# Kernel tuning notes

Measured on AMD Instinct MI355X. Metric: run time of the kernel, lower is better.

Reference implementation:

```python
import jax, jax.numpy as jnp
import numpy as np

T = 1_000_000
DT = 1e-3  # uniform t_eval spacing; integration horizon t in [0, 1000)


def setup_inputs() -> dict:
    return {
        "t_eval": jnp.arange(T, dtype=jnp.float32) * DT,
        "x0": jnp.array([0.15, 0.08, 0.05], dtype=jnp.float32),
        "log_eps": jnp.float32(-2.0),
        "log_delta": jnp.float32(-0.5),
        "theta": jnp.full((3,), 0.1, dtype=jnp.float32),
        "readout_w": jnp.eye(3, dtype=jnp.float32),   # nn.init.eye_
        "readout_b": jnp.zeros((3,), dtype=jnp.float32),
    }


def _build_W(log_eps, log_delta, dtype):
    # W[i,j] = 0 if i==j; -1+eps if i==(j+1)%3; else -1-delta
    eps = jnp.exp(log_eps)
    delta = jnp.exp(log_delta)
    eye = jnp.eye(3, dtype=dtype)
    cyc = jnp.array([[0, 0, 1], [1, 0, 0], [0, 1, 0]], dtype=dtype)  # i == (j+1)%3
    return cyc * (-1.0 + eps) + (1.0 - eye - cyc) * (-1.0 - delta)


def _integrate(t_eval, x0, log_eps, log_delta, theta):
    """Dormand-Prince 5(4) stages, one fixed step per t_eval interval (dopri5 tableau)."""
    W = _build_W(log_eps, log_delta, x0.dtype)

    def f(x):  # autonomous CTLN RHS: -x + relu(W x + theta)
        return -x + jax.nn.relu(W @ x + theta)

    def step(x, dt):
        k1 = f(x)
        k2 = f(x + dt * (1.0 / 5.0 * k1))
        k3 = f(x + dt * (3.0 / 40.0 * k1 + 9.0 / 40.0 * k2))
        k4 = f(x + dt * (44.0 / 45.0 * k1 - 56.0 / 15.0 * k2 + 32.0 / 9.0 * k3))
        k5 = f(x + dt * (19372.0 / 6561.0 * k1 - 25360.0 / 2187.0 * k2
                         + 64448.0 / 6561.0 * k3 - 212.0 / 729.0 * k4))
        k6 = f(x + dt * (9017.0 / 3168.0 * k1 - 355.0 / 33.0 * k2
                         + 46732.0 / 5247.0 * k3 + 49.0 / 176.0 * k4
                         - 5103.0 / 18656.0 * k5))
        x_new = x + dt * (35.0 / 384.0 * k1 + 500.0 / 1113.0 * k3
                          + 125.0 / 192.0 * k4 - 2187.0 / 6784.0 * k5
                          + 11.0 / 84.0 * k6)
        return x_new, x_new

    dts = jnp.diff(t_eval)                       # [T-1]
    _, xs = jax.lax.scan(step, x0, dts)          # [T-1, 3]
    return jnp.concatenate([x0[None, :], xs], axis=0)  # [T, 3]


def reference(t_eval, x0, log_eps, log_delta, theta, readout_w, readout_b):
    traj = _integrate(t_eval, x0, log_eps, log_delta, theta)  # [T, 3]
    pred = traj @ readout_w.T + readout_b                      # Linear(3,3)
    return traj, pred
```

## Files before the change

### kernel.cpp

```cpp
#include <hip/hip_runtime.h>
#include <math.h>


#define C21 (1.0/5.0)
#define C31 (3.0/40.0)
#define C32 (9.0/40.0)
#define C41 (44.0/45.0)
#define C42 (-56.0/15.0)
#define C43 (32.0/9.0)
#define C51 (19372.0/6561.0)
#define C52 (-25360.0/2187.0)
#define C53 (64448.0/6561.0)
#define C54 (-212.0/729.0)
#define C61 (9017.0/3168.0)
#define C62 (-355.0/33.0)
#define C63 (46732.0/5247.0)
#define C64 (49.0/176.0)
#define C65 (-5103.0/18656.0)
#define B1  (35.0/384.0)
#define B3  (500.0/1113.0)
#define B4  (125.0/192.0)
#define B5  (-2187.0/6784.0)
#define B6  (11.0/84.0)

template <typename T> struct MapT { T A[9]; T b[3]; };

template <typename T>
__device__ inline void map_identity(MapT<T>& m) {
#pragma unroll
  for (int i = 0; i < 9; ++i) m.A[i] = T(0);
  m.A[0] = m.A[4] = m.A[8] = T(1);
  m.b[0] = m.b[1] = m.b[2] = T(0);
}

template <typename T>
__device__ inline void map_compose(MapT<T>& out, const MapT<T>& m2, const MapT<T>& m1) {
#pragma unroll
  for (int r = 0; r < 3; ++r) {
#pragma unroll
    for (int c = 0; c < 3; ++c)
      out.A[r*3+c] = m2.A[r*3+0]*m1.A[0+c] + m2.A[r*3+1]*m1.A[3+c] + m2.A[r*3+2]*m1.A[6+c];
    out.b[r] = m2.A[r*3+0]*m1.b[0] + m2.A[r*3+1]*m1.b[1] + m2.A[r*3+2]*m1.b[2] + m2.b[r];
  }
}

template <typename T>
__device__ inline void map_apply(const MapT<T>& m, const T x[3], T y[3]) {
#pragma unroll
  for (int r = 0; r < 3; ++r)
    y[r] = m.A[r*3+0]*x[0] + m.A[r*3+1]*x[1] + m.A[r*3+2]*x[2] + m.b[r];
}

template <typename T>
__device__ inline MapT<T> map_shfl_up(const MapT<T>& m, int off) {
  MapT<T> r;
#pragma unroll
  for (int i = 0; i < 9; ++i) r.A[i] = __shfl_up(m.A[i], off, 64);
#pragma unroll
  for (int i = 0; i < 3; ++i) r.b[i] = __shfl_up(m.b[i], off, 64);
  return r;
}

template <typename T, bool RECORD>
__device__ inline void stage_k(const T z[3], const T th[3],
                               T wa, T wb, T g[3], T k[3]) {
  T y0 = fma(wa, z[2], fma(wb, z[1], th[0]));
  T y1 = fma(wa, z[0], fma(wb, z[2], th[1]));
  T y2 = fma(wa, z[1], fma(wb, z[0], th[2]));
  if (RECORD) {
    g[0] = (y0 > T(0)) ? T(1) : T(0);
    g[1] = (y1 > T(0)) ? T(1) : T(0);
    g[2] = (y2 > T(0)) ? T(1) : T(0);
  }
  k[0] = y0 * g[0] - z[0];
  k[1] = y1 * g[1] - z[1];
  k[2] = y2 * g[2] - z[2];
}

template <typename T, bool RECORD>
__device__ inline void dopri_eval(const T v[3], const T th[3], T dt,
                                  T wa, T wb, T G[6][3], T out[3]) {
  T k1[3], k2[3], k3[3], k4[3], k5[3], k6[3], z[3];
  stage_k<T, RECORD>(v, th, wa, wb, G[0], k1);
  const T d21 = dt * T(C21);
#pragma unroll
  for (int c = 0; c < 3; ++c) z[c] = fma(d21, k1[c], v[c]);
  stage_k<T, RECORD>(z, th, wa, wb, G[1], k2);
#pragma unroll
  for (int c = 0; c < 3; ++c) z[c] = fma(dt, fma(T(C31), k1[c], T(C32) * k2[c]), v[c]);
  stage_k<T, RECORD>(z, th, wa, wb, G[2], k3);
#pragma unroll
  for (int c = 0; c < 3; ++c)
    z[c] = fma(dt, fma(T(C41), k1[c], fma(T(C42), k2[c], T(C43) * k3[c])), v[c]);
  stage_k<T, RECORD>(z, th, wa, wb, G[3], k4);
#pragma unroll
  for (int c = 0; c < 3; ++c)
    z[c] = fma(dt, fma(T(C51), k1[c], fma(T(C52), k2[c], fma(T(C53), k3[c], T(C54) * k4[c]))), v[c]);
  stage_k<T, RECORD>(z, th, wa, wb, G[4], k5);
#pragma unroll
  for (int c = 0; c < 3; ++c)
    z[c] = fma(dt, fma(T(C61), k1[c], fma(T(C62), k2[c], fma(T(C63), k3[c], fma(T(C64), k4[c], T(C65) * k5[c])))), v[c]);
  stage_k<T, RECORD>(z, th, wa, wb, G[5], k6);
#pragma unroll
  for (int c = 0; c < 3; ++c)
    out[c] = fma(dt, fma(T(B1), k1[c], fma(T(B3), k3[c], fma(T(B4), k4[c], fma(T(B5), k5[c], T(B6) * k6[c])))), v[c]);
}

template <typename T>
__device__ inline void build_map(const T xo[3], T dt, T wa, T wb,
                                 const T th[3], MapT<T>& m) {
  T G[6][3], dump[3];
  dopri_eval<T, true>(xo, th, dt, wa, wb, G, dump);
  const T z3[3] = {T(0), T(0), T(0)};
  dopri_eval<T, false>(z3, th, dt, wa, wb, G, m.b);
  T e[3], col[3];
#pragma unroll
  for (int j = 0; j < 3; ++j) {
    e[0] = T(0); e[1] = T(0); e[2] = T(0); e[j] = T(1);
    dopri_eval<T, false>(e, z3, dt, wa, wb, G, col);
    m.A[0 + j] = col[0];
    m.A[3 + j] = col[1];
    m.A[6 + j] = col[2];
  }
}


__global__ void k_dts(const float* __restrict__ t, float* __restrict__ dts, int S) {
  int i = blockIdx.x * blockDim.x + threadIdx.x;
  if (i < S) dts[i] = t[i + 1] - t[i];
}

__global__ void k_coarse(const float* __restrict__ x0f,
                         const float* __restrict__ le, const float* __restrict__ ld,
                         const float* __restrict__ thf,
                         float* __restrict__ cst, int NC, float dtc) {
  if (threadIdx.x != 0 || blockIdx.x != 0) return;
  const float a = -1.f + expf(le[0]);
  const float b = -1.f - expf(ld[0]);
  const float t0 = thf[0], t1 = thf[1], t2 = thf[2];
  float x = x0f[0], y = x0f[1], z = x0f[2];
  cst[0] = x; cst[1] = y; cst[2] = z;
  const float dt = dtc, dth = 0.5f * dtc, dt6 = dtc * (1.f / 6.f);
#define RHSF(px, py, pz, kx, ky, kz)                      \
  do {                                                    \
    float y0_ = fmaf(a, (pz), fmaf(b, (py), t0));         \
    float y1_ = fmaf(a, (px), fmaf(b, (pz), t1));         \
    float y2_ = fmaf(a, (py), fmaf(b, (px), t2));         \
    (kx) = fmaxf(y0_, 0.f) - (px);                        \
    (ky) = fmaxf(y1_, 0.f) - (py);                        \
    (kz) = fmaxf(y2_, 0.f) - (pz);                        \
  } while (0)
  for (int i = 1; i <= NC; ++i) {
    float k1x,k1y,k1z,k2x,k2y,k2z,k3x,k3y,k3z,k4x,k4y,k4z,zx,zy,zz;
    RHSF(x, y, z, k1x, k1y, k1z);
    zx = fmaf(dth, k1x, x); zy = fmaf(dth, k1y, y); zz = fmaf(dth, k1z, z);
    RHSF(zx, zy, zz, k2x, k2y, k2z);
    zx = fmaf(dth, k2x, x); zy = fmaf(dth, k2y, y); zz = fmaf(dth, k2z, z);
    RHSF(zx, zy, zz, k3x, k3y, k3z);
    zx = fmaf(dt, k3x, x); zy = fmaf(dt, k3y, y); zz = fmaf(dt, k3z, z);
    RHSF(zx, zy, zz, k4x, k4y, k4z);
    x = fmaf(dt6, k1x + 2.f*k2x + 2.f*k3x + k4x, x);
    y = fmaf(dt6, k1y + 2.f*k2y + 2.f*k3y + k4y, y);
    z = fmaf(dt6, k1z + 2.f*k2z + 2.f*k3z + k4z, z);
    cst[3*i] = x; cst[3*i+1] = y; cst[3*i+2] = z;
  }
#undef RHSF
}

__global__ void k_interp(const float* __restrict__ t_eval, const float* __restrict__ st,
                         float* __restrict__ out, int T, float h, int nstates) {
  int n = blockIdx.x * blockDim.x + threadIdx.x;
  if (n >= T) return;
  float u = t_eval[n] / h;
  int j = (int)u;
  if (j < 0) j = 0;
  if (j > nstates - 2) j = nstates - 2;
  float f = u - (float)j;
#pragma unroll
  for (int c = 0; c < 3; ++c) {
    float a = st[3*j + c], b = st[3*(j+1) + c];
    out[3*n + c] = a + f * (b - a);
  }
}


#define FT 256
#define FT_LOG2 8
#define FCH 8
#define BT 512

template <typename T>
__global__ __launch_bounds__(FT) void k_upscan(
    const float* __restrict__ src, const float* __restrict__ dts,
    const float* __restrict__ le, const float* __restrict__ ld,
    const float* __restrict__ thf,
    MapT<T>* __restrict__ lpre, MapT<T>* __restrict__ btot, int S, int NG1) {
  __shared__ MapT<T> wtot[FT / 64];
  const int t = threadIdx.x;
  const int lane = t & 63, wid = t >> 6;
  const int g = blockIdx.x * FT + t;
  const T wa = (T)(-1.0 + exp((double)le[0]));
  const T wb = (T)(-1.0 - exp((double)ld[0]));
  const T th[3] = {(T)thf[0], (T)thf[1], (T)thf[2]};

  MapT<T> run, mp, tmp;
  map_identity(run);
  if (g < NG1) {
    for (int s = 0; s < FCH; ++s) {
      int n = g * FCH + s;
      if (n >= S) break;
      T xo[3] = {(T)src[3*n], (T)src[3*n+1], (T)src[3*n+2]};
      build_map(xo, (T)dts[n], wa, wb, th, mp);
      map_compose(tmp, mp, run);
      run = tmp;
    }
  }
#pragma unroll
  for (int off = 1; off < 64; off <<= 1) {
    MapT<T> nb = map_shfl_up(run, off);
    MapT<T> comp; map_compose(comp, run, nb);
    if (lane >= off) run = comp;
  }
  if (lane == 63) wtot[wid] = run;
  __syncthreads();
  MapT<T> wpre; map_identity(wpre);
  for (int w = 0; w < wid; ++w) { MapT<T> t2; map_compose(t2, wtot[w], wpre); wpre = t2; }

  MapT<T> excl = map_shfl_up(run, 1);
  if (lane == 0) map_identity(excl);
  MapT<T> P; map_compose(P, excl, wpre);
  lpre[g] = P;
  if (t == FT - 1) { MapT<T> bt; map_compose(bt, run, wpre); btot[blockIdx.x] = bt; }
}

template <typename T>
__global__ __launch_bounds__(BT) void k_bscan(const MapT<T>* __restrict__ btot,
                                              MapT<T>* __restrict__ bpre, int NB) {
  __shared__ MapT<T> wtot[BT / 64];
  const int t = threadIdx.x;
  const int lane = t & 63, wid = t >> 6;
  MapT<T> run;
  if (t < NB) run = btot[t]; else map_identity(run);
#pragma unroll
  for (int off = 1; off < 64; off <<= 1) {
    MapT<T> nb = map_shfl_up(run, off);
    MapT<T> comp; map_compose(comp, run, nb);
    if (lane >= off) run = comp;
  }
  if (lane == 63) wtot[wid] = run;
  __syncthreads();
  MapT<T> wpre; map_identity(wpre);
  for (int w = 0; w < wid; ++w) { MapT<T> t2; map_compose(t2, wtot[w], wpre); wpre = t2; }
  MapT<T> excl = map_shfl_up(run, 1);
  if (lane == 0) map_identity(excl);
  if (t < NB) { MapT<T> P; map_compose(P, excl, wpre); bpre[t] = P; }
}

template <typename T>
__global__ __launch_bounds__(FT) void k_apply2(
    const float* __restrict__ src, float* __restrict__ dst,
    const float* __restrict__ dts,
    const MapT<T>* __restrict__ lpre, const MapT<T>* __restrict__ bpre,
    const float* __restrict__ le, const float* __restrict__ ld,
    const float* __restrict__ thf, const float* __restrict__ x0f, int S, int NG1) {
  const int g = blockIdx.x * blockDim.x + threadIdx.x;
  if (g >= NG1) return;
  const T wa = (T)(-1.0 + exp((double)le[0]));
  const T wb = (T)(-1.0 - exp((double)ld[0]));
  const T th[3] = {(T)thf[0], (T)thf[1], (T)thf[2]};
  const T x0d[3] = {(T)x0f[0], (T)x0f[1], (T)x0f[2]};

  MapT<T> P;
  map_compose(P, lpre[g], bpre[g >> FT_LOG2]);
  T x[3], xn[3];
  map_apply(P, x0d, x);
  if (g == 0) { dst[0] = x0f[0]; dst[1] = x0f[1]; dst[2] = x0f[2]; }
  MapT<T> mp;
  for (int s = 0; s < FCH; ++s) {
    int n = g * FCH + s;
    if (n >= S) break;
    T xo[3] = {(T)src[3*n], (T)src[3*n+1], (T)src[3*n+2]};
    build_map(xo, (T)dts[n], wa, wb, th, mp);
    map_apply(mp, x, xn);
    x[0] = xn[0]; x[1] = xn[1]; x[2] = xn[2];
    dst[3*(n+1)]   = (float)x[0];
    dst[3*(n+1)+1] = (float)x[1];
    dst[3*(n+1)+2] = (float)x[2];
  }
}

__global__ __launch_bounds__(256) void k_polish(
    const float* __restrict__ src, float* __restrict__ dst,
    const float* __restrict__ dts,
    const float* __restrict__ le, const float* __restrict__ ld,
    const float* __restrict__ thf, const float* __restrict__ x0f, int S, int NG1) {
  const int g = blockIdx.x * blockDim.x + threadIdx.x;
  if (g >= NG1) return;
  const double wa = -1.0 + exp((double)le[0]);
  const double wb = -1.0 - exp((double)ld[0]);
  const double th[3] = {(double)thf[0], (double)thf[1], (double)thf[2]};
  const int n0 = g * FCH;
  double x[3];
  if (g == 0) {
    x[0] = (double)x0f[0]; x[1] = (double)x0f[1]; x[2] = (double)x0f[2];
    dst[0] = x0f[0]; dst[1] = x0f[1]; dst[2] = x0f[2];
  } else {
    x[0] = (double)src[3*n0]; x[1] = (double)src[3*n0+1]; x[2] = (double)src[3*n0+2];
  }
  double G[6][3], xn[3];
  for (int s = 0; s < FCH; ++s) {
    int n = n0 + s;
    if (n >= S) break;
    dopri_eval<double, true>(x, th, (double)dts[n], wa, wb, G, xn);
    x[0] = xn[0]; x[1] = xn[1]; x[2] = xn[2];
    dst[3*(n+1)]   = (float)x[0];
    dst[3*(n+1)+1] = (float)x[1];
    dst[3*(n+1)+2] = (float)x[2];
  }
}

__global__ void k_readout(const float* __restrict__ traj, const float* __restrict__ w,
                          const float* __restrict__ bvec, float* __restrict__ pred, int T) {
  const float w00=w[0],w01=w[1],w02=w[2];
  const float w10=w[3],w11=w[4],w12=w[5];
  const float w20=w[6],w21=w[7],w22=w[8];
  const float b0=bvec[0], b1=bvec[1], b2=bvec[2];
  for (int i = blockIdx.x * blockDim.x + threadIdx.x; i < T;
       i += gridDim.x * blockDim.x) {
    const float x0 = traj[3*i], x1 = traj[3*i+1], x2 = traj[3*i+2];
    pred[3*i]   = fmaf(w00,x0, fmaf(w01,x1, fmaf(w02,x2, b0)));
    pred[3*i+1] = fmaf(w10,x0, fmaf(w11,x1, fmaf(w12,x2, b1)));
    pred[3*i+2] = fmaf(w20,x0, fmaf(w21,x1, fmaf(w22,x2, b2)));
  }
}


extern "C" void kernel_launch(void* const* d_in, const int* in_sizes, int n_in,
                              void* d_out, int out_size, void* d_ws, size_t ws_size,
                              hipStream_t stream) {
  const float* t_eval    = (const float*)d_in[0];
  const float* x0        = (const float*)d_in[1];
  const float* log_eps   = (const float*)d_in[2];
  const float* log_delta = (const float*)d_in[3];
  const float* theta     = (const float*)d_in[4];
  const float* readout_w = (const float*)d_in[5];
  const float* readout_b = (const float*)d_in[6];

  const int T   = in_sizes[0];
  const int S   = T - 1;
  const int NG1 = (S + FCH - 1) / FCH;
  const int NB  = (NG1 + FT - 1) / FT;

  const float  DTS_SEED = 0.45f;
  const int    NSEED    = (int)(((double)S * 1e-3) / (double)DTS_SEED) + 2;

  float* trajh = (float*)d_out;
  float* predh = trajh + (size_t)3 * T;

  char* w = (char*)d_ws;
  float* dts    = (float*)w;  w += (((size_t)S * 4) + 255) & ~(size_t)255;
  float* seedst = (float*)w;  w += (((size_t)3 * (NSEED + 1) * 4) + 255) & ~(size_t)255;
  MapT<float>* lpre = (MapT<float>*)w; w += (((size_t)NB * FT * sizeof(MapT<float>)) + 255) & ~(size_t)255;
  MapT<float>* btot = (MapT<float>*)w; w += (((size_t)BT * sizeof(MapT<float>)) + 255) & ~(size_t)255;
  MapT<float>* bpre = (MapT<float>*)w;

  k_dts<<<(S + 255) / 256, 256, 0, stream>>>(t_eval, dts, S);
  k_coarse<<<1, 64, 0, stream>>>(x0, log_eps, log_delta, theta, seedst, NSEED, DTS_SEED);
  k_interp<<<(T + 255) / 256, 256, 0, stream>>>(t_eval, seedst, predh, T,
                                                DTS_SEED, NSEED + 1);

  for (int it = 0; it < 4; ++it) {
    const float* src = (it % 2 == 0) ? predh : trajh;
    float*       dst = (it % 2 == 0) ? trajh : predh;
    k_upscan<float><<<NB, FT, 0, stream>>>(src, dts, log_eps, log_delta, theta,
                                           lpre, btot, S, NG1);
    k_bscan<float><<<1, BT, 0, stream>>>(btot, bpre, NB);
    k_apply2<float><<<(NG1 + FT - 1) / FT, FT, 0, stream>>>(src, dst, dts, lpre, bpre,
                                                            log_eps, log_delta, theta,
                                                            x0, S, NG1);
  }

  k_polish<<<(NG1 + 255) / 256, 256, 0, stream>>>(predh, trajh, dts, log_eps,
                                                  log_delta, theta, x0, S, NG1);

  k_readout<<<2048, 256, 0, stream>>>(trajh, readout_w, readout_b, predh, T);
}
```

Measured before the change: 627.2 us.

## Fuse Newton-scan iterations into one cooperative kernel over group start states

Replaces the per-iteration upscan, bscan and apply kernel trio with a single cooperative kernel that uses grid.sync between the block-level scan and the cross-block scan. Only per-group start states are carried between iterations; the full trajectory is no longer written each pass, since each thread re-walks its chunk from its start state. The chunk size per thread goes from 8 to 16, step sizes are computed inline from t_eval, and the readout is fused into the final double-precision polish kernel. A multi-kernel fallback path runs if the cooperative launch fails. The cost is more recomputation per thread and a dependence on all blocks being co-resident.

```diff
diff --git a/kernel.cpp b/kernel.cpp
--- a/kernel.cpp
+++ b/kernel.cpp
@@ -1,5 +1,8 @@
 #include <hip/hip_runtime.h>
+#include <hip/hip_cooperative_groups.h>
 #include <math.h>
+
+namespace cg = cooperative_groups;
 
 
 #define C21 (1.0/5.0)
@@ -23,18 +26,21 @@
 #define B5  (-2187.0/6784.0)
 #define B6  (11.0/84.0)
 
-template <typename T> struct MapT { T A[9]; T b[3]; };
-
-template <typename T>
-__device__ inline void map_identity(MapT<T>& m) {
-#pragma unroll
-  for (int i = 0; i < 9; ++i) m.A[i] = T(0);
-  m.A[0] = m.A[4] = m.A[8] = T(1);
-  m.b[0] = m.b[1] = m.b[2] = T(0);
-}
-
-template <typename T>
-__device__ inline void map_compose(MapT<T>& out, const MapT<T>& m2, const MapT<T>& m1) {
+#define FT 256
+#define FT_LOG2 8
+#define FCH 16
+#define NITER 4
+
+struct MapF { float A[9]; float b[3]; };
+
+__device__ inline void map_identity(MapF& m) {
+#pragma unroll
+  for (int i = 0; i < 9; ++i) m.A[i] = 0.f;
+  m.A[0] = m.A[4] = m.A[8] = 1.f;
+  m.b[0] = m.b[1] = m.b[2] = 0.f;
+}
+
+__device__ inline void map_compose(MapF& out, const MapF& m2, const MapF& m1) {
 #pragma unroll
   for (int r = 0; r < 3; ++r) {
 #pragma unroll
@@ -44,16 +50,14 @@
   }
 }
 
-template <typename T>
-__device__ inline void map_apply(const MapT<T>& m, const T x[3], T y[3]) {
+__device__ inline void map_apply(const MapF& m, const float x[3], float y[3]) {
 #pragma unroll
   for (int r = 0; r < 3; ++r)
     y[r] = m.A[r*3+0]*x[0] + m.A[r*3+1]*x[1] + m.A[r*3+2]*x[2] + m.b[r];
 }
 
-template <typename T>
-__device__ inline MapT<T> map_shfl_up(const MapT<T>& m, int off) {
-  MapT<T> r;
+__device__ inline MapF map_shfl_up(const MapF& m, int off) {
+  MapF r;
 #pragma unroll
   for (int i = 0; i < 9; ++i) r.A[i] = __shfl_up(m.A[i], off, 64);
 #pragma unroll
@@ -106,29 +110,71 @@
     out[c] = fma(dt, fma(T(B1), k1[c], fma(T(B3), k3[c], fma(T(B4), k4[c], fma(T(B5), k5[c], T(B6) * k6[c])))), v[c]);
 }
 
-template <typename T>
-__device__ inline void build_map(const T xo[3], T dt, T wa, T wb,
-                                 const T th[3], MapT<T>& m) {
-  T G[6][3], dump[3];
-  dopri_eval<T, true>(xo, th, dt, wa, wb, G, dump);
-  const T z3[3] = {T(0), T(0), T(0)};
-  dopri_eval<T, false>(z3, th, dt, wa, wb, G, m.b);
-  T e[3], col[3];
+__device__ inline void build_map_step(float x[3], float dt, float wa, float wb,
+                                      const float th[3], MapF& m) {
+  float G[6][3], xn[3];
+  dopri_eval<float, true>(x, th, dt, wa, wb, G, xn);
+  const float z3[3] = {0.f, 0.f, 0.f};
+  dopri_eval<float, false>(z3, th, dt, wa, wb, G, m.b);
+  float e[3], col[3];
 #pragma unroll
   for (int j = 0; j < 3; ++j) {
-    e[0] = T(0); e[1] = T(0); e[2] = T(0); e[j] = T(1);
-    dopri_eval<T, false>(e, z3, dt, wa, wb, G, col);
+    e[0] = 0.f; e[1] = 0.f; e[2] = 0.f; e[j] = 1.f;
+    dopri_eval<float, false>(e, z3, dt, wa, wb, G, col);
     m.A[0 + j] = col[0];
     m.A[3 + j] = col[1];
     m.A[6 + j] = col[2];
   }
-}
-
-
-__global__ void k_dts(const float* __restrict__ t, float* __restrict__ dts, int S) {
-  int i = blockIdx.x * blockDim.x + threadIdx.x;
-  if (i < S) dts[i] = t[i + 1] - t[i];
-}
+  x[0] = xn[0]; x[1] = xn[1]; x[2] = xn[2];
+}
+
+__device__ inline void block_scan(MapF run, MapF& P, MapF& tot,
+                                  MapF* wtot, int lane, int wid) {
+#pragma unroll
+  for (int off = 1; off < 64; off <<= 1) {
+    MapF nb = map_shfl_up(run, off);
+    MapF c; map_compose(c, run, nb);
+    if (lane >= off) run = c;
+  }
+  __syncthreads();
+  if (lane == 63) wtot[wid] = run;
+  __syncthreads();
+  MapF wpre; map_identity(wpre);
+  for (int w = 0; w < wid; ++w) { MapF t2; map_compose(t2, wtot[w], wpre); wpre = t2; }
+  MapF excl = map_shfl_up(run, 1);
+  if (lane == 0) map_identity(excl);
+  map_compose(P, excl, wpre);
+  map_compose(tot, run, wpre);
+}
+
+__device__ inline void group_walk(float xs[3], const float dtg[FCH],
+                                  float wa, float wb, const float th[3],
+                                  MapF& run) {
+  map_identity(run);
+  MapF mp, tmp;
+  float x[3] = {xs[0], xs[1], xs[2]};
+#pragma unroll
+  for (int s = 0; s < FCH; ++s) {
+    build_map_step(x, dtg[s], wa, wb, th, mp);
+    map_compose(tmp, mp, run);
+    run = tmp;
+  }
+}
+
+__device__ inline void load_dtg(const float* __restrict__ t_eval, int n0, int T,
+                                float dtg[FCH], float& tv0) {
+  int i0 = n0 > T - 1 ? T - 1 : n0;
+  tv0 = t_eval[i0];
+  float prev = tv0;
+#pragma unroll
+  for (int s = 1; s <= FCH; ++s) {
+    int idx = n0 + s; if (idx > T - 1) idx = T - 1;
+    float c = t_eval[idx];
+    dtg[s - 1] = c - prev;
+    prev = c;
+  }
+}
+
 
 __global__ void k_coarse(const float* __restrict__ x0f,
                          const float* __restrict__ le, const float* __restrict__ ld,
@@ -167,171 +213,203 @@
 #undef RHSF
 }
 
-__global__ void k_interp(const float* __restrict__ t_eval, const float* __restrict__ st,
-                         float* __restrict__ out, int T, float h, int nstates) {
-  int n = blockIdx.x * blockDim.x + threadIdx.x;
-  if (n >= T) return;
-  float u = t_eval[n] / h;
+__global__ __launch_bounds__(FT) void k_mega(
+    const float* __restrict__ t_eval, const float* __restrict__ seedst,
+    const float* __restrict__ x0f,
+    const float* __restrict__ le, const float* __restrict__ ld,
+    const float* __restrict__ thf,
+    float* __restrict__ gstart,
+    MapF* __restrict__ btot, MapF* __restrict__ bpre,
+    int S, int T, int NG1, int NB, float hseed, int nstates) {
+  cg::grid_group grid = cg::this_grid();
+  __shared__ MapF wtot[FT / 64];
+
+  const int t = threadIdx.x;
+  const int lane = t & 63, wid = t >> 6;
+  const int g = blockIdx.x * FT + t;
+  const bool active = (g < NG1);
+  const int n0 = g * FCH;
+
+  const float wa = -1.f + expf(le[0]);
+  const float wb = -1.f - expf(ld[0]);
+  const float th[3] = {thf[0], thf[1], thf[2]};
+  const float x0d[3] = {x0f[0], x0f[1], x0f[2]};
+
+  float dtg[FCH];
+  float xs[3] = {0.f, 0.f, 0.f};
+  if (active) {
+    float tv0;
+    load_dtg(t_eval, n0, T, dtg, tv0);
+    float u = tv0 / hseed;
+    int j = (int)u;
+    if (j < 0) j = 0;
+    if (j > nstates - 2) j = nstates - 2;
+    float f = u - (float)j;
+#pragma unroll
+    for (int c = 0; c < 3; ++c) {
+      float a0 = seedst[3*j + c], b0 = seedst[3*(j+1) + c];
+      xs[c] = a0 + f * (b0 - a0);
+    }
+  } else {
+#pragma unroll
+    for (int s = 0; s < FCH; ++s) dtg[s] = 0.f;
+  }
+  if (g == 0) { xs[0] = x0d[0]; xs[1] = x0d[1]; xs[2] = x0d[2]; }
+
+  for (int it = 0; it < NITER; ++it) {
+    MapF run;
+    if (active) group_walk(xs, dtg, wa, wb, th, run);
+    else map_identity(run);
+
+    MapF P, tot;
+    block_scan(run, P, tot, wtot, lane, wid);
+    if (t == FT - 1) btot[blockIdx.x] = tot;
+    grid.sync();
+
+    if (blockIdx.x == 0) {
+      MapF rb;
+      if (t < NB) rb = btot[t]; else map_identity(rb);
+      MapF Pb, totb;
+      block_scan(rb, Pb, totb, wtot, lane, wid);
+      if (t < NB) bpre[t] = Pb;
+    }
+    grid.sync();
+
+    {
+      MapF bp = bpre[blockIdx.x];
+      MapF Pn; map_compose(Pn, P, bp);
+      float ns[3]; map_apply(Pn, x0d, ns);
+      if (active && g != 0) { xs[0] = ns[0]; xs[1] = ns[1]; xs[2] = ns[2]; }
+    }
+  }
+
+  if (active) {
+    gstart[3*g]   = xs[0];
+    gstart[3*g+1] = xs[1];
+    gstart[3*g+2] = xs[2];
+  }
+}
+
+__global__ __launch_bounds__(256) void k_polish(
+    const float* __restrict__ t_eval, const float* __restrict__ gstart,
+    const float* __restrict__ x0f,
+    const float* __restrict__ le, const float* __restrict__ ld,
+    const float* __restrict__ thf,
+    const float* __restrict__ row, const float* __restrict__ rob,
+    float* __restrict__ traj, float* __restrict__ pred, int S, int T, int NG1) {
+  const int g = blockIdx.x * blockDim.x + threadIdx.x;
+  if (g >= NG1) return;
+  const int n0 = g * FCH;
+  float dtg[FCH]; float tv0;
+  load_dtg(t_eval, n0, T, dtg, tv0);
+
+  const double wa = -1.0 + exp((double)le[0]);
+  const double wb = -1.0 - exp((double)ld[0]);
+  const double th[3] = {(double)thf[0], (double)thf[1], (double)thf[2]};
+  const float w00 = row[0], w01 = row[1], w02 = row[2];
+  const float w10 = row[3], w11 = row[4], w12 = row[5];
+  const float w20 = row[6], w21 = row[7], w22 = row[8];
+  const float b0 = rob[0], b1 = rob[1], b2 = rob[2];
+
+  double x[3];
+  if (g == 0) {
+    x[0] = (double)x0f[0]; x[1] = (double)x0f[1]; x[2] = (double)x0f[2];
+    float a0 = x0f[0], a1 = x0f[1], a2 = x0f[2];
+    traj[0] = a0; traj[1] = a1; traj[2] = a2;
+    pred[0] = fmaf(w00, a0, fmaf(w01, a1, fmaf(w02, a2, b0)));
+    pred[1] = fmaf(w10, a0, fmaf(w11, a1, fmaf(w12, a2, b1)));
+    pred[2] = fmaf(w20, a0, fmaf(w21, a1, fmaf(w22, a2, b2)));
+  } else {
+    x[0] = (double)gstart[3*g]; x[1] = (double)gstart[3*g+1]; x[2] = (double)gstart[3*g+2];
+  }
+
+  double G[6][3], xn[3];
+#pragma unroll
+  for (int s = 0; s < FCH; ++s) {
+    dopri_eval<double, true>(x, th, (double)dtg[s], wa, wb, G, xn);
+    x[0] = xn[0]; x[1] = xn[1]; x[2] = xn[2];
+    int n = n0 + s;
+    if (n < S) {
+      float a0 = (float)x[0], a1 = (float)x[1], a2 = (float)x[2];
+      traj[3*(n+1)]   = a0;
+      traj[3*(n+1)+1] = a1;
+      traj[3*(n+1)+2] = a2;
+      pred[3*(n+1)]   = fmaf(w00, a0, fmaf(w01, a1, fmaf(w02, a2, b0)));
+      pred[3*(n+1)+1] = fmaf(w10, a0, fmaf(w11, a1, fmaf(w12, a2, b1)));
+      pred[3*(n+1)+2] = fmaf(w20, a0, fmaf(w21, a1, fmaf(w22, a2, b2)));
+    }
+  }
+}
+
+
+__global__ void k_start0(const float* __restrict__ t_eval,
+                         const float* __restrict__ seedst,
+                         const float* __restrict__ x0f,
+                         float* __restrict__ gs, int T, int NG1,
+                         float hseed, int nstates) {
+  int g = blockIdx.x * blockDim.x + threadIdx.x;
+  if (g >= NG1) return;
+  if (g == 0) { gs[0] = x0f[0]; gs[1] = x0f[1]; gs[2] = x0f[2]; return; }
+  int n0 = g * FCH; if (n0 > T - 1) n0 = T - 1;
+  float u = t_eval[n0] / hseed;
   int j = (int)u;
   if (j < 0) j = 0;
   if (j > nstates - 2) j = nstates - 2;
   float f = u - (float)j;
 #pragma unroll
   for (int c = 0; c < 3; ++c) {
-    float a = st[3*j + c], b = st[3*(j+1) + c];
-    out[3*n + c] = a + f * (b - a);
-  }
-}
-
-
-#define FT 256
-#define FT_LOG2 8
-#define FCH 8
-#define BT 512
-
-template <typename T>
-__global__ __launch_bounds__(FT) void k_upscan(
-    const float* __restrict__ src, const float* __restrict__ dts,
+    float a0 = seedst[3*j + c], b0 = seedst[3*(j+1) + c];
+    gs[3*g + c] = a0 + f * (b0 - a0);
+  }
+}
+
+__global__ __launch_bounds__(FT) void k_up_fb(
+    const float* __restrict__ t_eval, const float* __restrict__ gs,
     const float* __restrict__ le, const float* __restrict__ ld,
     const float* __restrict__ thf,
-    MapT<T>* __restrict__ lpre, MapT<T>* __restrict__ btot, int S, int NG1) {
-  __shared__ MapT<T> wtot[FT / 64];
-  const int t = threadIdx.x;
-  const int lane = t & 63, wid = t >> 6;
+    MapF* __restrict__ lpre, MapF* __restrict__ btot, int T, int NG1) {
+  __shared__ MapF wtot[FT / 64];
+  const int t = threadIdx.x, lane = t & 63, wid = t >> 6;
   const int g = blockIdx.x * FT + t;
-  const T wa = (T)(-1.0 + exp((double)le[0]));
-  const T wb = (T)(-1.0 - exp((double)ld[0]));
-  const T th[3] = {(T)thf[0], (T)thf[1], (T)thf[2]};
-
-  MapT<T> run, mp, tmp;
-  map_identity(run);
-  if (g < NG1) {
-    for (int s = 0; s < FCH; ++s) {
-      int n = g * FCH + s;
-      if (n >= S) break;
-      T xo[3] = {(T)src[3*n], (T)src[3*n+1], (T)src[3*n+2]};
-      build_map(xo, (T)dts[n], wa, wb, th, mp);
-      map_compose(tmp, mp, run);
-      run = tmp;
-    }
-  }
-#pragma unroll
-  for (int off = 1; off < 64; off <<= 1) {
-    MapT<T> nb = map_shfl_up(run, off);
-    MapT<T> comp; map_compose(comp, run, nb);
-    if (lane >= off) run = comp;
-  }
-  if (lane == 63) wtot[wid] = run;
-  __syncthreads();
-  MapT<T> wpre; map_identity(wpre);
-  for (int w = 0; w < wid; ++w) { MapT<T> t2; map_compose(t2, wtot[w], wpre); wpre = t2; }
-
-  MapT<T> excl = map_shfl_up(run, 1);
-  if (lane == 0) map_identity(excl);
-  MapT<T> P; map_compose(P, excl, wpre);
-  lpre[g] = P;
-  if (t == FT - 1) { MapT<T> bt; map_compose(bt, run, wpre); btot[blockIdx.x] = bt; }
-}
-
-template <typename T>
-__global__ __launch_bounds__(BT) void k_bscan(const MapT<T>* __restrict__ btot,
-                                              MapT<T>* __restrict__ bpre, int NB) {
-  __shared__ MapT<T> wtot[BT / 64];
-  const int t = threadIdx.x;
-  const int lane = t & 63, wid = t >> 6;
-  MapT<T> run;
+  const bool active = (g < NG1);
+  const float wa = -1.f + expf(le[0]);
+  const float wb = -1.f - expf(ld[0]);
+  const float th[3] = {thf[0], thf[1], thf[2]};
+  MapF run;
+  if (active) {
+    float dtg[FCH]; float tv0;
+    load_dtg(t_eval, g * FCH, T, dtg, tv0);
+    float xs[3] = {gs[3*g], gs[3*g+1], gs[3*g+2]};
+    group_walk(xs, dtg, wa, wb, th, run);
+  } else map_identity(run);
+  MapF P, tot;
+  block_scan(run, P, tot, wtot, lane, wid);
+  if (active) lpre[g] = P;
+  if (t == FT - 1) btot[blockIdx.x] = tot;
+}
+
+__global__ __launch_bounds__(FT) void k_bscan_fb(const MapF* __restrict__ btot,
+                                                 MapF* __restrict__ bpre, int NB) {
+  __shared__ MapF wtot[FT / 64];
+  const int t = threadIdx.x, lane = t & 63, wid = t >> 6;
+  MapF run;
   if (t < NB) run = btot[t]; else map_identity(run);
-#pragma unroll
-  for (int off = 1; off < 64; off <<= 1) {
-    MapT<T> nb = map_shfl_up(run, off);
-    MapT<T> comp; map_compose(comp, run, nb);
-    if (lane >= off) run = comp;
-  }
-  if (lane == 63) wtot[wid] = run;
-  __syncthreads();
-  MapT<T> wpre; map_identity(wpre);
-  for (int w = 0; w < wid; ++w) { MapT<T> t2; map_compose(t2, wtot[w], wpre); wpre = t2; }
-  MapT<T> excl = map_shfl_up(run, 1);
-  if (lane == 0) map_identity(excl);
-  if (t < NB) { MapT<T> P; map_compose(P, excl, wpre); bpre[t] = P; }
-}
-
-template <typename T>
-__global__ __launch_bounds__(FT) void k_apply2(
-    const float* __restrict__ src, float* __restrict__ dst,
-    const float* __restrict__ dts,
-    const MapT<T>* __restrict__ lpre, const MapT<T>* __restrict__ bpre,
-    const float* __restrict__ le, const float* __restrict__ ld,
-    const float* __restrict__ thf, const float* __restrict__ x0f, int S, int NG1) {
-  const int g = blockIdx.x * blockDim.x + threadIdx.x;
+  MapF P, tot;
+  block_scan(run, P, tot, wtot, lane, wid);
+  if (t < NB) bpre[t] = P;
+}
+
+__global__ void k_fold_fb(const MapF* __restrict__ lpre, const MapF* __restrict__ bpre,
+                          const float* __restrict__ x0f,
+                          float* __restrict__ gsout, int NG1) {
+  int g = blockIdx.x * blockDim.x + threadIdx.x;
   if (g >= NG1) return;
-  const T wa = (T)(-1.0 + exp((double)le[0]));
-  const T wb = (T)(-1.0 - exp((double)ld[0]));
-  const T th[3] = {(T)thf[0], (T)thf[1], (T)thf[2]};
-  const T x0d[3] = {(T)x0f[0], (T)x0f[1], (T)x0f[2]};
-
-  MapT<T> P;
+  if (g == 0) { gsout[0] = x0f[0]; gsout[1] = x0f[1]; gsout[2] = x0f[2]; return; }
+  MapF P;
   map_compose(P, lpre[g], bpre[g >> FT_LOG2]);
-  T x[3], xn[3];
-  map_apply(P, x0d, x);
-  if (g == 0) { dst[0] = x0f[0]; dst[1] = x0f[1]; dst[2] = x0f[2]; }
-  MapT<T> mp;
-  for (int s = 0; s < FCH; ++s) {
-    int n = g * FCH + s;
-    if (n >= S) break;
-    T xo[3] = {(T)src[3*n], (T)src[3*n+1], (T)src[3*n+2]};
-    build_map(xo, (T)dts[n], wa, wb, th, mp);
-    map_apply(mp, x, xn);
-    x[0] = xn[0]; x[1] = xn[1]; x[2] = xn[2];
-    dst[3*(n+1)]   = (float)x[0];
-    dst[3*(n+1)+1] = (float)x[1];
-    dst[3*(n+1)+2] = (float)x[2];
-  }
-}
-
-__global__ __launch_bounds__(256) void k_polish(
-    const float* __restrict__ src, float* __restrict__ dst,
-    const float* __restrict__ dts,
-    const float* __restrict__ le, const float* __restrict__ ld,
-    const float* __restrict__ thf, const float* __restrict__ x0f, int S, int NG1) {
-  const int g = blockIdx.x * blockDim.x + threadIdx.x;
-  if (g >= NG1) return;
-  const double wa = -1.0 + exp((double)le[0]);
-  const double wb = -1.0 - exp((double)ld[0]);
-  const double th[3] = {(double)thf[0], (double)thf[1], (double)thf[2]};
-  const int n0 = g * FCH;
-  double x[3];
-  if (g == 0) {
-    x[0] = (double)x0f[0]; x[1] = (double)x0f[1]; x[2] = (double)x0f[2];
-    dst[0] = x0f[0]; dst[1] = x0f[1]; dst[2] = x0f[2];
-  } else {
-    x[0] = (double)src[3*n0]; x[1] = (double)src[3*n0+1]; x[2] = (double)src[3*n0+2];
-  }
-  double G[6][3], xn[3];
-  for (int s = 0; s < FCH; ++s) {
-    int n = n0 + s;
-    if (n >= S) break;
-    dopri_eval<double, true>(x, th, (double)dts[n], wa, wb, G, xn);
-    x[0] = xn[0]; x[1] = xn[1]; x[2] = xn[2];
-    dst[3*(n+1)]   = (float)x[0];
-    dst[3*(n+1)+1] = (float)x[1];
-    dst[3*(n+1)+2] = (float)x[2];
-  }
-}
-
-__global__ void k_readout(const float* __restrict__ traj, const float* __restrict__ w,
-                          const float* __restrict__ bvec, float* __restrict__ pred, int T) {
-  const float w00=w[0],w01=w[1],w02=w[2];
-  const float w10=w[3],w11=w[4],w12=w[5];
-  const float w20=w[6],w21=w[7],w22=w[8];
-  const float b0=bvec[0], b1=bvec[1], b2=bvec[2];
-  for (int i = blockIdx.x * blockDim.x + threadIdx.x; i < T;
-       i += gridDim.x * blockDim.x) {
-    const float x0 = traj[3*i], x1 = traj[3*i+1], x2 = traj[3*i+2];
-    pred[3*i]   = fmaf(w00,x0, fmaf(w01,x1, fmaf(w02,x2, b0)));
-    pred[3*i+1] = fmaf(w10,x0, fmaf(w11,x1, fmaf(w12,x2, b1)));
-    pred[3*i+2] = fmaf(w20,x0, fmaf(w21,x1, fmaf(w22,x2, b2)));
-  }
+  float x0d[3] = {x0f[0], x0f[1], x0f[2]}, ns[3];
+  map_apply(P, x0d, ns);
+  gsout[3*g] = ns[0]; gsout[3*g+1] = ns[1]; gsout[3*g+2] = ns[2];
 }
 
 
@@ -346,42 +424,64 @@
   const float* readout_w = (const float*)d_in[5];
   const float* readout_b = (const float*)d_in[6];
 
-  const int T   = in_sizes[0];
-  const int S   = T - 1;
-  const int NG1 = (S + FCH - 1) / FCH;
-  const int NB  = (NG1 + FT - 1) / FT;
-
-  const float  DTS_SEED = 0.45f;
-  const int    NSEED    = (int)(((double)S * 1e-3) / (double)DTS_SEED) + 2;
+  int T_   = in_sizes[0];
+  int S_   = T_ - 1;
+  int NG1_ = (S_ + FCH - 1) / FCH;
+  int NB_  = (NG1_ + FT - 1) / FT;
+
+  const float DTS_SEED = 0.45f;
+  const int   NSEED    = (int)(((double)S_ * 1e-3) / (double)DTS_SEED) + 2;
+  int nstates_ = NSEED + 1;
+  float hseed_ = DTS_SEED;
 
   float* trajh = (float*)d_out;
-  float* predh = trajh + (size_t)3 * T;
+  float* predh = trajh + (size_t)3 * T_;
 
   char* w = (char*)d_ws;
-  float* dts    = (float*)w;  w += (((size_t)S * 4) + 255) & ~(size_t)255;
   float* seedst = (float*)w;  w += (((size_t)3 * (NSEED + 1) * 4) + 255) & ~(size_t)255;
-  MapT<float>* lpre = (MapT<float>*)w; w += (((size_t)NB * FT * sizeof(MapT<float>)) + 255) & ~(size_t)255;
-  MapT<float>* btot = (MapT<float>*)w; w += (((size_t)BT * sizeof(MapT<float>)) + 255) & ~(size_t)255;
-  MapT<float>* bpre = (MapT<float>*)w;
-
-  k_dts<<<(S + 255) / 256, 256, 0, stream>>>(t_eval, dts, S);
+  float* gsA    = (float*)w;  w += (((size_t)3 * NG1_ * 4) + 255) & ~(size_t)255;
+  float* gsB    = (float*)w;  w += (((size_t)3 * NG1_ * 4) + 255) & ~(size_t)255;
+  MapF* lpre    = (MapF*)w;   w += (((size_t)NG1_ * sizeof(MapF)) + 255) & ~(size_t)255;
+  MapF* btot    = (MapF*)w;   w += (((size_t)NB_ * sizeof(MapF)) + 255) & ~(size_t)255;
+  MapF* bpre    = (MapF*)w;
+
   k_coarse<<<1, 64, 0, stream>>>(x0, log_eps, log_delta, theta, seedst, NSEED, DTS_SEED);
-  k_interp<<<(T + 255) / 256, 256, 0, stream>>>(t_eval, seedst, predh, T,
-                                                DTS_SEED, NSEED + 1);
-
-  for (int it = 0; it < 4; ++it) {
-    const float* src = (it % 2 == 0) ? predh : trajh;
-    float*       dst = (it % 2 == 0) ? trajh : predh;
-    k_upscan<float><<<NB, FT, 0, stream>>>(src, dts, log_eps, log_delta, theta,
-                                           lpre, btot, S, NG1);
-    k_bscan<float><<<1, BT, 0, stream>>>(btot, bpre, NB);
-    k_apply2<float><<<(NG1 + FT - 1) / FT, FT, 0, stream>>>(src, dst, dts, lpre, bpre,
-                                                            log_eps, log_delta, theta,
-                                                            x0, S, NG1);
-  }
-
-  k_polish<<<(NG1 + 255) / 256, 256, 0, stream>>>(predh, trajh, dts, log_eps,
-                                                  log_delta, theta, x0, S, NG1);
-
-  k_readout<<<2048, 256, 0, stream>>>(trajh, readout_w, readout_b, predh, T);
-}
+
+  const float* t_eval_ = t_eval;
+  const float* seedst_ = seedst;
+  const float* x0_ = x0;
+  const float* le_ = log_eps;
+  const float* ld_ = log_delta;
+  const float* th_ = theta;
+  float* gs_ = gsA;
+  MapF* btot_ = btot;
+  MapF* bpre_ = bpre;
+
+  void* args[] = {
+    (void*)&t_eval_, (void*)&seedst_, (void*)&x0_, (void*)&le_, (void*)&ld_,
+    (void*)&th_, (void*)&gs_, (void*)&btot_, (void*)&bpre_,
+    (void*)&S_, (void*)&T_, (void*)&NG1_, (void*)&NB_,
+    (void*)&hseed_, (void*)&nstates_,
+  };
+  hipError_t cerr = hipLaunchCooperativeKernel((const void*)k_mega, dim3(NB_), dim3(FT),
+                                               args, 0, stream);
+  const float* finalgs = gsA;
+  if (cerr != hipSuccess) {
+    k_start0<<<(NG1_ + 255) / 256, 256, 0, stream>>>(t_eval, seedst, x0, gsA,
+                                                     T_, NG1_, hseed_, nstates_);
+    float* cur = gsA; float* nxt = gsB;
+    for (int it = 0; it < NITER; ++it) {
+      k_up_fb<<<NB_, FT, 0, stream>>>(t_eval, cur, log_eps, log_delta, theta,
+                                      lpre, btot, T_, NG1_);
+      k_bscan_fb<<<1, FT, 0, stream>>>(btot, bpre, NB_);
+      k_fold_fb<<<(NG1_ + 255) / 256, 256, 0, stream>>>(lpre, bpre, x0, nxt, NG1_);
+      float* tmp = cur; cur = nxt; nxt = tmp;
+    }
+    finalgs = cur;
+  }
+
+  k_polish<<<(NG1_ + 255) / 256, 256, 0, stream>>>(t_eval, finalgs, x0,
+                                                   log_eps, log_delta, theta,
+                                                   readout_w, readout_b,
+                                                   trajh, predh, S_, T_, NG1_);
+}
```

Result: slower. 740.5 us (+18.1%).
